# Kernel optimization log

Hardware: AMD Instinct MI355X
Metric: run time of the kernel (lower is better)

## Reference

```python
import jax, jax.numpy as jnp
import numpy as np

K = 4096   # infeatures
N = 8192   # outfeatures
M = 8192   # tokens (batch*seq)
GROUPSIZE = 128
PACK = 8   # int4 values per int32


def setup_inputs() -> dict:
    key = jax.random.key(0)
    k1, k2, k3 = jax.random.split(key, 3)
    A = jax.random.normal(k1, (M, K), dtype=jnp.float32)
    # packed int4 weights: 8 nibbles per int32 along k -> shape (K//8, N)
    B_packed = jax.random.randint(k2, (K // PACK, N), 0, 2147483647, dtype=jnp.int32)
    # positive per-group scales, shape (K//groupsize, N)
    s = jax.random.uniform(k3, (K // GROUPSIZE, N), dtype=jnp.float32,
                           minval=0.001, maxval=0.02)
    return {"A": A, "B_packed": B_packed, "s": s}


def reference(A, B_packed, s):
    # Unpack int4 nibbles: q in [0, 15], zero-point = 8 (symmetric quantization,
    # matches pack(): w = round(w/s) + 8, clamp [0, 15]).
    k = A.shape[-1]
    groups, n = s.shape
    gs = k // groups
    shifts = (jnp.arange(PACK, dtype=jnp.int32) * 4)
    q = (B_packed[:, None, :] >> shifts[None, :, None]) & 0xF        # (k//8, 8, n)
    q = q.reshape(k, n).astype(A.dtype)
    # dequantize with per-group scales, then dense GEMM: C = A @ W
    W = ((q - 8.0).reshape(groups, gs, n) * s[:, None, :]).reshape(k, n)
    return A @ W
```

## Files before the change

### kernel.cpp

```cpp
#include <hip/hip_runtime.h>


typedef _Float16 h2 __attribute__((ext_vector_type(2)));
typedef _Float16 h8 __attribute__((ext_vector_type(8)));
typedef float f32x4 __attribute__((ext_vector_type(4)));

#define MM 8192
#define NN 8192
#define KK 4096

__global__ __launch_bounds__(512, 2) void w4a32_gemm(
    const float* __restrict__ A, const int* __restrict__ Bq,
    const float* __restrict__ S, float* __restrict__ C)
{
  extern __shared__ __align__(16) char smem[];
  const int tid  = threadIdx.x;
  const int lane = tid & 63;
  const int wid  = tid >> 6;
  const int wm   = wid >> 2;
  const int wn   = wid & 3;
  const int ln15 = lane & 15;
  const int l16  = lane >> 4;

  const int bid = blockIdx.x;
  const int swz = (bid & 7) * 128 + (bid >> 3);
  const int bm  = swz >> 5;
  const int bn  = swz & 31;

  const int am  = tid >> 1;
  const int akh = tid & 1;
  const float* Ap = A + (size_t)(bm * 256 + am) * KK + akh * 32;

  const int bkp = tid & 7;
  const int bn4 = (tid >> 3) << 2;
  const int*   Bp = Bq + (size_t)bkp * NN + bn * 256 + bn4;
  const float* Sp = S + bn * 256 + bn4;

  int awoff[4], bwoff[4];
#pragma unroll
  for (int j = 0; j < 4; ++j)
    awoff[j] = (am * 128 + (akh * 4 + j) * 16) ^ ((am & 7) << 4);
#pragma unroll
  for (int i = 0; i < 4; ++i)
    bwoff[i] = ((bn4 + i) * 128 + bkp * 16) ^ (((bn4 + i) & 7) << 4);

  f32x4 acc[8][4];
#pragma unroll
  for (int mi = 0; mi < 8; ++mi)
#pragma unroll
    for (int ni = 0; ni < 4; ++ni)
      acc[mi][ni] = (f32x4){0.f, 0.f, 0.f, 0.f};

  float4 av[8]; int4 wq; float4 sv;

  auto load_stage = [&](int koff) {
    const float4* ap = (const float4*)(Ap + koff);
#pragma unroll
    for (int j = 0; j < 8; ++j) av[j] = ap[j];
    wq = *(const int4*)(Bp + (size_t)(koff >> 6) * (8 * NN));
    sv = *(const float4*)(Sp + (size_t)(koff >> 7) * NN);
  };

  auto write_stage = [&](char* sa, char* sb) {
#pragma unroll
    for (int j = 0; j < 4; ++j) {
      float4 f0 = av[2 * j], f1 = av[2 * j + 1];
      auto p0 = __builtin_amdgcn_cvt_pkrtz(f0.x, f1.x);
      auto p1 = __builtin_amdgcn_cvt_pkrtz(f0.y, f1.y);
      auto p2 = __builtin_amdgcn_cvt_pkrtz(f0.z, f1.z);
      auto p3 = __builtin_amdgcn_cvt_pkrtz(f0.w, f1.w);
      int4 wd;
      wd.x = __builtin_bit_cast(int, p0);
      wd.y = __builtin_bit_cast(int, p1);
      wd.z = __builtin_bit_cast(int, p2);
      wd.w = __builtin_bit_cast(int, p3);
      *(int4*)(sa + awoff[j]) = wd;
    }
    const h2 cM = {(_Float16)(-1032.f), (_Float16)(-1032.f)};
#pragma unroll
    for (int i = 0; i < 4; ++i) {
      unsigned w = (unsigned)((i == 0) ? wq.x : (i == 1) ? wq.y : (i == 2) ? wq.z : wq.w);
      float   sc = (i == 0) ? sv.x : (i == 1) ? sv.y : (i == 2) ? sv.z : sv.w;
      _Float16 sh = (_Float16)sc;
      h2 s2 = {sh, sh};
      unsigned x0 = ( w        & 0x000F000Fu) | 0x64006400u;
      unsigned x1 = ((w >> 4)  & 0x000F000Fu) | 0x64006400u;
      unsigned x2 = ((w >> 8)  & 0x000F000Fu) | 0x64006400u;
      unsigned x3 = ((w >> 12) & 0x000F000Fu) | 0x64006400u;
      h2 r0 = (__builtin_bit_cast(h2, x0) + cM) * s2;
      h2 r1 = (__builtin_bit_cast(h2, x1) + cM) * s2;
      h2 r2 = (__builtin_bit_cast(h2, x2) + cM) * s2;
      h2 r3 = (__builtin_bit_cast(h2, x3) + cM) * s2;
      int4 wd;
      wd.x = __builtin_bit_cast(int, r0);
      wd.y = __builtin_bit_cast(int, r1);
      wd.z = __builtin_bit_cast(int, r2);
      wd.w = __builtin_bit_cast(int, r3);
      *(int4*)(sb + bwoff[i]) = wd;
    }
  };

  auto compute = [&](const char* sa, const char* sb) {
#pragma unroll
    for (int ks = 0; ks < 2; ++ks) {
      h8 bf[4];
#pragma unroll
      for (int ni = 0; ni < 4; ++ni) {
        int row = wn * 64 + ni * 16 + ln15;
        int off = (row * 128 + (ks * 4 + l16) * 16) ^ ((row & 7) << 4);
        bf[ni] = *(const h8*)(sb + off);
      }
#pragma unroll
      for (int mi = 0; mi < 8; ++mi) {
        int row = wm * 128 + mi * 16 + ln15;
        int off = (row * 128 + (ks * 4 + l16) * 16) ^ ((row & 7) << 4);
        h8 af = *(const h8*)(sa + off);
#pragma unroll
        for (int ni = 0; ni < 4; ++ni)
          acc[mi][ni] = __builtin_amdgcn_mfma_f32_16x16x32_f16(af, bf[ni], acc[mi][ni], 0, 0, 0);
      }
    }
  };

  load_stage(0);
  write_stage(smem, smem + 32768);
  __syncthreads();

  int cur = 0;
  for (int t = 0; t < 63; ++t) {
    load_stage((t + 1) * 64);
    compute(smem + cur * 65536, smem + cur * 65536 + 32768);
    int nxt = cur ^ 1;
    write_stage(smem + nxt * 65536, smem + nxt * 65536 + 32768);
    __syncthreads();
    cur = nxt;
  }
  compute(smem + cur * 65536, smem + cur * 65536 + 32768);

  float* Cp = C + (size_t)(bm * 256 + wm * 128) * NN + bn * 256 + wn * 64;
#pragma unroll
  for (int mi = 0; mi < 8; ++mi)
#pragma unroll
    for (int ni = 0; ni < 4; ++ni)
#pragma unroll
      for (int j = 0; j < 4; ++j)
        Cp[(size_t)(mi * 16 + l16 * 4 + j) * NN + ni * 16 + ln15] = acc[mi][ni][j];
}

extern "C" void kernel_launch(void* const* d_in, const int* in_sizes, int n_in,
                              void* d_out, int out_size, void* d_ws, size_t ws_size,
                              hipStream_t stream) {
  const float* A  = (const float*)d_in[0];
  const int*   Bq = (const int*)d_in[1];
  const float* S  = (const float*)d_in[2];
  float* C = (float*)d_out;

  (void)hipFuncSetAttribute((const void*)w4a32_gemm,
                            hipFuncAttributeMaxDynamicSharedMemorySize, 131072);

  dim3 grid(1024), block(512);
  w4a32_gemm<<<grid, block, 131072, stream>>>(A, Bq, S, C);
}
```

Before: 1.268 ms.

## Interleave global loads, LDS writes and MFMA clusters with barriers and setprio

Each k-iteration's compute is split into four MFMA clusters. The next stage's A load, B load, A LDS write and B dequant/write are spread between them, and s_barrier plus s_setprio(1) keep the waves of a block in step and give MFMA work priority. This aims to overlap memory and VALU work with matrix ops instead of running them in separate phases. It adds extra workgroup barriers per iteration and may raise register pressure. A wave's LDS writes to the next buffer can also run while other waves are still reading the current one; this is safe only because the buffers are distinct.

```diff
diff --git a/kernel.cpp b/kernel.cpp
--- a/kernel.cpp
+++ b/kernel.cpp
@@ -53,15 +53,17 @@
 
   float4 av[8]; int4 wq; float4 sv;
 
-  auto load_stage = [&](int koff) {
+  auto load_A = [&](int koff) {
     const float4* ap = (const float4*)(Ap + koff);
 #pragma unroll
     for (int j = 0; j < 8; ++j) av[j] = ap[j];
+  };
+  auto load_B = [&](int koff) {
     wq = *(const int4*)(Bp + (size_t)(koff >> 6) * (8 * NN));
     sv = *(const float4*)(Sp + (size_t)(koff >> 7) * NN);
   };
 
-  auto write_stage = [&](char* sa, char* sb) {
+  auto write_A = [&](char* sa) {
 #pragma unroll
     for (int j = 0; j < 4; ++j) {
       float4 f0 = av[2 * j], f1 = av[2 * j + 1];
@@ -76,6 +78,9 @@
       wd.w = __builtin_bit_cast(int, p3);
       *(int4*)(sa + awoff[j]) = wd;
     }
+  };
+
+  auto write_B = [&](char* sb) {
     const h2 cM = {(_Float16)(-1032.f), (_Float16)(-1032.f)};
 #pragma unroll
     for (int i = 0; i < 4; ++i) {
@@ -100,42 +105,87 @@
     }
   };
 
-  auto compute = [&](const char* sa, const char* sb) {
-#pragma unroll
-    for (int ks = 0; ks < 2; ++ks) {
-      h8 bf[4];
-#pragma unroll
-      for (int ni = 0; ni < 4; ++ni) {
-        int row = wn * 64 + ni * 16 + ln15;
-        int off = (row * 128 + (ks * 4 + l16) * 16) ^ ((row & 7) << 4);
-        bf[ni] = *(const h8*)(sb + off);
-      }
-#pragma unroll
-      for (int mi = 0; mi < 8; ++mi) {
-        int row = wm * 128 + mi * 16 + ln15;
-        int off = (row * 128 + (ks * 4 + l16) * 16) ^ ((row & 7) << 4);
-        h8 af = *(const h8*)(sa + off);
-#pragma unroll
-        for (int ni = 0; ni < 4; ++ni)
-          acc[mi][ni] = __builtin_amdgcn_mfma_f32_16x16x32_f16(af, bf[ni], acc[mi][ni], 0, 0, 0);
-      }
-    }
-  };
-
-  load_stage(0);
-  write_stage(smem, smem + 32768);
+  auto read_af = [&](const char* sa, int mi, int ks) -> h8 {
+    int row = wm * 128 + mi * 16 + ln15;
+    int off = (row * 128 + (ks * 4 + l16) * 16) ^ ((row & 7) << 4);
+    return *(const h8*)(sa + off);
+  };
+  auto read_bf = [&](const char* sb, int ni, int ks) -> h8 {
+    int row = wn * 64 + ni * 16 + ln15;
+    int off = (row * 128 + (ks * 4 + l16) * 16) ^ ((row & 7) << 4);
+    return *(const h8*)(sb + off);
+  };
+
+  load_A(0); load_B(0);
+  write_A(smem); write_B(smem + 32768);
   __syncthreads();
 
   int cur = 0;
-  for (int t = 0; t < 63; ++t) {
-    load_stage((t + 1) * 64);
-    compute(smem + cur * 65536, smem + cur * 65536 + 32768);
-    int nxt = cur ^ 1;
-    write_stage(smem + nxt * 65536, smem + nxt * 65536 + 32768);
+  for (int t = 0; t < 64; ++t) {
+    char* sa = smem + cur * 65536;
+    char* sb = sa + 32768;
+    char* na = smem + (cur ^ 1) * 65536;
+    char* nb = na + 32768;
+    const bool pre = (t < 63);
+    h8 af[4], bf[4];
+
+#pragma unroll
+    for (int mi = 0; mi < 4; ++mi) af[mi] = read_af(sa, mi, 0);
+#pragma unroll
+    for (int ni = 0; ni < 4; ++ni) bf[ni] = read_bf(sb, ni, 0);
+    if (pre) load_A((t + 1) * 64);
+    __builtin_amdgcn_s_barrier();
+    __builtin_amdgcn_s_setprio(1);
+#pragma unroll
+    for (int mi = 0; mi < 4; ++mi)
+#pragma unroll
+      for (int ni = 0; ni < 4; ++ni)
+        acc[mi][ni] = __builtin_amdgcn_mfma_f32_16x16x32_f16(af[mi], bf[ni], acc[mi][ni], 0, 0, 0);
+    __builtin_amdgcn_s_setprio(0);
+    __builtin_amdgcn_s_barrier();
+
+#pragma unroll
+    for (int mi = 0; mi < 4; ++mi) af[mi] = read_af(sa, mi + 4, 0);
+    if (pre) load_B((t + 1) * 64);
+    __builtin_amdgcn_s_barrier();
+    __builtin_amdgcn_s_setprio(1);
+#pragma unroll
+    for (int mi = 0; mi < 4; ++mi)
+#pragma unroll
+      for (int ni = 0; ni < 4; ++ni)
+        acc[mi + 4][ni] = __builtin_amdgcn_mfma_f32_16x16x32_f16(af[mi], bf[ni], acc[mi + 4][ni], 0, 0, 0);
+    __builtin_amdgcn_s_setprio(0);
+    __builtin_amdgcn_s_barrier();
+
+#pragma unroll
+    for (int mi = 0; mi < 4; ++mi) af[mi] = read_af(sa, mi, 1);
+#pragma unroll
+    for (int ni = 0; ni < 4; ++ni) bf[ni] = read_bf(sb, ni, 1);
+    if (pre) write_A(na);
+    __builtin_amdgcn_s_barrier();
+    __builtin_amdgcn_s_setprio(1);
+#pragma unroll
+    for (int mi = 0; mi < 4; ++mi)
+#pragma unroll
+      for (int ni = 0; ni < 4; ++ni)
+        acc[mi][ni] = __builtin_amdgcn_mfma_f32_16x16x32_f16(af[mi], bf[ni], acc[mi][ni], 0, 0, 0);
+    __builtin_amdgcn_s_setprio(0);
+    __builtin_amdgcn_s_barrier();
+
+#pragma unroll
+    for (int mi = 0; mi < 4; ++mi) af[mi] = read_af(sa, mi + 4, 1);
+    if (pre) write_B(nb);
+    __builtin_amdgcn_s_barrier();
+    __builtin_amdgcn_s_setprio(1);
+#pragma unroll
+    for (int mi = 0; mi < 4; ++mi)
+#pragma unroll
+      for (int ni = 0; ni < 4; ++ni)
+        acc[mi + 4][ni] = __builtin_amdgcn_mfma_f32_16x16x32_f16(af[mi], bf[ni], acc[mi + 4][ni], 0, 0, 0);
+    __builtin_amdgcn_s_setprio(0);
     __syncthreads();
-    cur = nxt;
+    cur ^= 1;
   }
-  compute(smem + cur * 65536, smem + cur * 65536 + 32768);
 
   float* Cp = C + (size_t)(bm * 256 + wm * 128) * NN + bn * 256 + wn * 64;
 #pragma unroll
```

Measured after the change: 1.320 ms. 4.1% more time.
